# Kernel optimization log

Hardware: AMD Instinct MI355X
Metric: run time of the kernel (lower is better)

## Reference

```python
import jax, jax.numpy as jnp
import numpy as np

B, N, D, H, DH, E, BIAS_DIM = 8, 512, 512, 8, 64, 32768, 8

def setup_inputs() -> dict:
    key = jax.random.key(0)
    ks = jax.random.split(key, 10)
    states = jax.random.normal(ks[0], (B, N, D), jnp.float32)
    key_states = jax.random.normal(ks[1], (B, N, D), jnp.float32)
    # causal mask, broadcastable over heads: [B,1,N,N]
    masks = jnp.broadcast_to(jnp.tril(jnp.ones((N, N), jnp.float32)), (B, 1, N, N))
    edge_type = jax.random.randint(ks[2], (E, 1), 0, BIAS_DIM, jnp.int32)
    b_idx = jax.random.randint(ks[3], (E, 1), 0, B, jnp.int32)
    q_idx = jax.random.randint(ks[4], (E, 1), 0, N, jnp.int32)
    k_idx = jax.random.randint(ks[5], (E, 1), 0, N, jnp.int32)
    attention_bias = jnp.concatenate([edge_type, b_idx, q_idx, k_idx], axis=1)
    s = 0.05
    Wq = jax.random.normal(ks[6], (D, H, DH), jnp.float32) * s
    Wk = jax.random.normal(ks[7], (D, H, DH), jnp.float32) * s
    Wv = jax.random.normal(ks[8], (D, H, DH), jnp.float32) * s
    k2 = jax.random.split(ks[9], 3)
    Wo = jax.random.normal(k2[0], (H, DH, D), jnp.float32) * s
    bias_embs = jax.random.normal(k2[1], (BIAS_DIM, DH), jnp.float32) * s
    bias_scalar = jax.random.normal(k2[2], (DH, 1), jnp.float32) * s
    return {"states": states, "key_states": key_states, "masks": masks,
            "attention_bias": attention_bias, "Wq": Wq, "Wk": Wk, "Wv": Wv,
            "Wo": Wo, "bias_embs": bias_embs, "bias_scalar": bias_scalar}

def reference(states, key_states, masks, attention_bias, Wq, Wk, Wv, Wo, bias_embs, bias_scalar):
    q = jnp.einsum('btd,dha->btha', states, Wq)
    k = jnp.einsum('btd,dha->btha', key_states, Wk)
    v = jnp.einsum('btd,dha->btha', key_states, Wv)
    alpha = jnp.einsum('bkha,bqha->bhqk', k, q)  # [B,H,Q,K]
    # sparse edge bias: embed edge types, project to scalar, scatter into [B,Q,K]
    et = attention_bias[:, 0]
    bias_vals = (bias_embs[et] @ bias_scalar)[:, 0]  # [E]
    bq, bk = alpha.shape[2], alpha.shape[3]
    bias_mat = jnp.zeros((alpha.shape[0], bq, bk), alpha.dtype)
    bias_mat = bias_mat.at[attention_bias[:, 1], attention_bias[:, 2], attention_bias[:, 3]].add(bias_vals)
    summed_keys = jnp.sum(k, axis=-1)  # [B,K,H]
    alpha = alpha + jnp.einsum('bqk,bkh->bhqk', bias_mat, summed_keys)
    alpha = alpha * jax.lax.rsqrt(jnp.float32(DH))
    neg = jnp.finfo(jnp.float32).min
    alpha = alpha * masks + (1.0 - jnp.ceil(masks)) * neg
    alpha = jax.nn.softmax(alpha, axis=-1)
    alpha = alpha * masks
    context = jnp.einsum('bhqk,bkha->bqha', alpha, v)
    return jnp.einsum('btha,had->btd', context, Wo)
```

## Files before the change

kernel.cpp:

```cpp
#include <hip/hip_runtime.h>

typedef unsigned short u16;
typedef unsigned int u32;
typedef __bf16 bf16x8 __attribute__((ext_vector_type(8)));
typedef float f32x4 __attribute__((ext_vector_type(4)));
typedef u16 u16x8 __attribute__((ext_vector_type(8)));
typedef u16 u16x4 __attribute__((ext_vector_type(4)));


__device__ __forceinline__ u16 f2b(float f) {
  union { float f; u32 i; } v; v.f = f;
  u32 r = v.i + 0x7fffu + ((v.i >> 16) & 1u);
  return (u16)(r >> 16);
}

#define GLL16(gp, lp)                                                      \
  __builtin_amdgcn_global_load_lds(                                       \
      (const __attribute__((address_space(1))) u32*)(gp),                 \
      (__attribute__((address_space(3))) u32*)(lp), 16, 0, 0)

__device__ __forceinline__ void stage64(const u16* g, u16* l, int wave, int lane) {
  int rsub = lane >> 3;
  int gs = (((lane & 7) ^ rsub) << 3);
  #pragma unroll
  for (int c = 0; c < 2; c++) {
    int ch = wave * 2 + c;
    GLL16(g + (size_t)(ch * 8 + rsub) * 512 + gs, l + ch * 512);
  }
}
__device__ __forceinline__ void stage128(const u16* g, u16* l, int wave, int lane) {
  int rsub = lane >> 3;
  int gs = (((lane & 7) ^ rsub) << 3);
  #pragma unroll
  for (int c = 0; c < 4; c++) {
    int ch = wave * 4 + c;
    GLL16(g + (size_t)(ch * 8 + rsub) * 512 + gs, l + ch * 512);
  }
}
__device__ __forceinline__ int swz(int row, int g) {
  return row * 64 + ((g ^ (row & 7)) << 3);
}

__global__ __launch_bounds__(256) void wprep(
    const float* __restrict__ Wq, const float* __restrict__ Wk,
    const float* __restrict__ Wv, const float* __restrict__ Wo,
    u16* __restrict__ wbase, float* __restrict__ bias_mat) {
  __shared__ u16 t[32][33];
  int bid = blockIdx.x;
  int tid = threadIdx.x;
  if (bid < 1024) {
    int z = bid >> 8, rem = bid & 255;
    int bx = rem & 15, by = rem >> 4;
    const float* src; float sc = 1.f;
    if (z == 0)      { src = Wq; sc = 0.125f; }
    else if (z == 1) { src = Wk; }
    else if (z == 2) { src = Wv; }
    else             { src = Wo; }
    u16* dst = wbase + (size_t)z * 262144;
    int tx = tid & 31, ty = tid >> 5;
    int c0 = bx * 32, r0 = by * 32;
    #pragma unroll
    for (int i = ty; i < 32; i += 8) t[i][tx] = f2b(src[(r0 + i) * 512 + c0 + tx] * sc);
    __syncthreads();
    #pragma unroll
    for (int i = ty; i < 32; i += 8) dst[(c0 + i) * 512 + r0 + tx] = t[tx][i];
  } else {
    int i = (bid - 1024) * 256 + tid;
    float4 z4 = {0.f, 0.f, 0.f, 0.f};
    ((float4*)bias_mat)[i] = z4;
  }
}

__global__ __launch_bounds__(256) void qkv_gemm(const float* __restrict__ states,
                                                const float* __restrict__ key_states,
                                                const u16* __restrict__ wT,
                                                const int* __restrict__ ab,
                                                const float* __restrict__ be,
                                                const float* __restrict__ bsc,
                                                float* __restrict__ bias_m,
                                                u16* __restrict__ qb,
                                                u16* __restrict__ kbo,
                                                u16* __restrict__ vtb,
                                                float* __restrict__ summed,
                                                int n_edges) {
  __shared__ alignas(16) u16 As[2][64 * 64];
  __shared__ alignas(16) u16 Bs[2][128 * 64];
  __shared__ float ssum[4][64];
  __shared__ float tvs[8];
  int tid = threadIdx.x;
  int lane = tid & 63, wave = tid >> 6;
  int quad = lane >> 4, ln = lane & 15;
  int fb = blockIdx.y * 64 + blockIdx.x;

  if (tid < 8) {
    const float4* bev = (const float4*)(be + tid * 64);
    const float4* bscv = (const float4*)bsc;
    float s = 0.f;
    #pragma unroll
    for (int a4 = 0; a4 < 16; a4++) {
      float4 x = bev[a4], y = bscv[a4];
      s += x.x * y.x + x.y * y.y + x.z * y.z + x.w * y.w;
    }
    tvs[tid] = s * 0.125f;
  }
  __syncthreads();
  for (int e = fb * 256 + tid; e < n_edges; e += 768 * 256) {
    int et = ab[e * 4 + 0];
    int b  = ab[e * 4 + 1];
    int qi = ab[e * 4 + 2];
    int ki = ab[e * 4 + 3];
    if (ki <= qi)
      atomicAdd(&bias_m[((size_t)b * 512 + qi) * 512 + ki], tvs[et]);
  }

  int row0 = blockIdx.x * 64;
  int col0 = blockIdx.y * 128;
  const float* A = (col0 < 512) ? states : key_states;
  const u16* Bb = wT + (size_t)col0 * 512;

  int ar = tid >> 2, aj = tid & 3;
  const float* apA = A + (size_t)(row0 + ar) * 512 + aj * 16;

  f32x4 acc[4][2];
  #pragma unroll
  for (int i = 0; i < 4; i++)
    #pragma unroll
    for (int j = 0; j < 2; j++) acc[i][j] = (f32x4){0.f, 0.f, 0.f, 0.f};

  float4 rA[4];
  {
    const float4* p = (const float4*)apA;
    rA[0] = p[0]; rA[1] = p[1]; rA[2] = p[2]; rA[3] = p[3];
  }
  stage128(Bb, Bs[0], wave, lane);

  int cur = 0;
  for (int k0 = 0; k0 < 512; k0 += 64) {
    __syncthreads();
    {
      u16x8 q0, q1;
      q0[0]=f2b(rA[0].x); q0[1]=f2b(rA[0].y); q0[2]=f2b(rA[0].z); q0[3]=f2b(rA[0].w);
      q0[4]=f2b(rA[1].x); q0[5]=f2b(rA[1].y); q0[6]=f2b(rA[1].z); q0[7]=f2b(rA[1].w);
      q1[0]=f2b(rA[2].x); q1[1]=f2b(rA[2].y); q1[2]=f2b(rA[2].z); q1[3]=f2b(rA[2].w);
      q1[4]=f2b(rA[3].x); q1[5]=f2b(rA[3].y); q1[6]=f2b(rA[3].z); q1[7]=f2b(rA[3].w);
      *(u16x8*)&As[cur][swz(ar, 2 * aj)]     = q0;
      *(u16x8*)&As[cur][swz(ar, 2 * aj + 1)] = q1;
    }
    __syncthreads();
    if (k0 < 448) {
      stage128(Bb + k0 + 64, Bs[cur ^ 1], wave, lane);
      const float4* p = (const float4*)(apA + k0 + 64);
      rA[0] = p[0]; rA[1] = p[1]; rA[2] = p[2]; rA[3] = p[3];
    }
    #pragma unroll
    for (int s = 0; s < 2; s++) {
      bf16x8 af[4], bfv[2];
      #pragma unroll
      for (int i = 0; i < 4; i++)
        af[i] = *(bf16x8*)&As[cur][swz(i * 16 + ln, s * 4 + quad)];
      #pragma unroll
      for (int j = 0; j < 2; j++)
        bfv[j] = *(bf16x8*)&Bs[cur][swz(wave * 32 + j * 16 + ln, s * 4 + quad)];
      #pragma unroll
      for (int i = 0; i < 4; i++)
        #pragma unroll
        for (int j = 0; j < 2; j++)
          acc[i][j] = __builtin_amdgcn_mfma_f32_16x16x32_bf16(af[i], bfv[j], acc[i][j], 0, 0, 0);
    }
    cur ^= 1;
  }

  int region = col0 >> 9;
  int nbase = col0 & 511;
  if (region <= 1) {
    u16* Cout = region ? kbo : qb;
    #pragma unroll
    for (int i = 0; i < 4; i++)
      #pragma unroll
      for (int j = 0; j < 2; j++) {
        int mb = row0 + i * 16 + quad * 4;
        int n = nbase + wave * 32 + j * 16 + ln;
        #pragma unroll
        for (int r = 0; r < 4; r++)
          Cout[(size_t)(mb + r) * 512 + n] = f2b(acc[i][j][r]);
      }
    if (region == 1) {
      #pragma unroll
      for (int i = 0; i < 4; i++)
        #pragma unroll
        for (int r = 0; r < 4; r++) {
          float v = acc[i][0][r] + acc[i][1][r];
          v += __shfl_xor(v, 1);
          v += __shfl_xor(v, 2);
          v += __shfl_xor(v, 4);
          v += __shfl_xor(v, 8);
          if (ln == 0) ssum[wave][i * 16 + quad * 4 + r] = v;
        }
      __syncthreads();
      if (tid < 128) {
        int hl = tid >> 6, row = tid & 63;
        float s = ssum[hl * 2][row] + ssum[hl * 2 + 1][row];
        int m = row0 + row;
        int b = m >> 9, t = m & 511;
        int h = (nbase >> 6) + hl;
        summed[((size_t)(b * 8 + h)) * 512 + t] = s;
      }
    }
  } else {
    #pragma unroll
    for (int i = 0; i < 4; i++)
      #pragma unroll
      for (int j = 0; j < 2; j++) {
        int mb = row0 + i * 16 + quad * 4;
        int bb = mb >> 9, t0 = mb & 511;
        int a_abs = nbase + wave * 32 + j * 16 + ln;
        int h = a_abs >> 6, a = a_abs & 63;
        u16x4 p;
        p[0] = f2b(acc[i][j][0]); p[1] = f2b(acc[i][j][1]);
        p[2] = f2b(acc[i][j][2]); p[3] = f2b(acc[i][j][3]);
        *(u16x4*)&vtb[(((size_t)bb * 8 + h) * 64 + a) * 512 + t0] = p;
      }
  }
}

__global__ __launch_bounds__(256) void attn_mfma(const u16* __restrict__ q,
                                                 const u16* __restrict__ k,
                                                 const u16* __restrict__ vt,
                                                 const float* __restrict__ bias_mat,
                                                 const float* __restrict__ summed,
                                                 u16* __restrict__ ctx) {
  __shared__ alignas(16) u16 Qs[64 * 64];
  __shared__ alignas(16) u16 Ks[2][64 * 64];
  __shared__ alignas(16) u16 Vs[2][64 * 64];
  __shared__ alignas(16) u16 Ps[4][16 * 72];
  int tid = threadIdx.x;
  int wave = tid >> 6, lane = tid & 63;
  int quad = lane >> 4, ln = lane & 15;
  int p2 = blockIdx.x;
  int bh, qt;
  if (p2 < 256) { bh = p2 & 63; qt = 7 - (p2 >> 6); }
  else          { int q2 = p2 - 256; bh = q2 & 63; qt = q2 >> 6; }
  int b = bh >> 3, h = bh & 7;
  int q0 = qt * 64;
  int kbe = qt;

  const u16* qb_ = q + ((size_t)(b * 512 + q0)) * 512 + h * 64;
  const u16* kb_ = k + ((size_t)(b * 512)) * 512 + h * 64;
  const u16* vb_ = vt + ((size_t)bh * 64) * 512;

  stage64(qb_, Qs, wave, lane);
  stage64(kb_, Ks[0], wave, lane);
  stage64(vb_, Vs[0], wave, lane);

  float m_r[4], l_r[4];
  f32x4 o[4];
  #pragma unroll
  for (int r = 0; r < 4; r++) { m_r[r] = -3.40282347e38f; l_r[r] = 0.f; }
  #pragma unroll
  for (int nt = 0; nt < 4; nt++) o[nt] = (f32x4){0.f, 0.f, 0.f, 0.f};

  int qrow = q0 + wave * 16 + quad * 4;

  float c_skv[4], c_bias[4][4];
  #pragma unroll
  for (int nt = 0; nt < 4; nt++) {
    int t = nt * 16 + ln;
    c_skv[nt] = summed[bh * 512 + t];
    const float* bp2 = bias_mat + ((size_t)(b * 512 + qrow)) * 512 + t;
    #pragma unroll
    for (int r = 0; r < 4; r++) c_bias[nt][r] = bp2[(size_t)r * 512];
  }

  int cur = 0;
  for (int kb = 0; kb <= kbe; kb++) {
    __syncthreads();

    float n_skv[4], n_bias[4][4];
    if (kb < kbe) {
      stage64(kb_ + (size_t)(kb + 1) * 64 * 512, Ks[cur ^ 1], wave, lane);
      stage64(vb_ + (kb + 1) * 64, Vs[cur ^ 1], wave, lane);
      #pragma unroll
      for (int nt = 0; nt < 4; nt++) {
        int t = (kb + 1) * 64 + nt * 16 + ln;
        n_skv[nt] = summed[bh * 512 + t];
        const float* bp2 = bias_mat + ((size_t)(b * 512 + qrow)) * 512 + t;
        #pragma unroll
        for (int r = 0; r < 4; r++) n_bias[nt][r] = bp2[(size_t)r * 512];
      }
    }

    bf16x8 aq0 = *(bf16x8*)&Qs[swz(wave * 16 + ln, quad)];
    bf16x8 aq1 = *(bf16x8*)&Qs[swz(wave * 16 + ln, 4 + quad)];
    f32x4 s[4];
    #pragma unroll
    for (int nt = 0; nt < 4; nt++) {
      bf16x8 b0 = *(bf16x8*)&Ks[cur][swz(nt * 16 + ln, quad)];
      bf16x8 b1 = *(bf16x8*)&Ks[cur][swz(nt * 16 + ln, 4 + quad)];
      s[nt] = (f32x4){0.f, 0.f, 0.f, 0.f};
      s[nt] = __builtin_amdgcn_mfma_f32_16x16x32_bf16(aq0, b0, s[nt], 0, 0, 0);
      s[nt] = __builtin_amdgcn_mfma_f32_16x16x32_bf16(aq1, b1, s[nt], 0, 0, 0);
    }

    #pragma unroll
    for (int nt = 0; nt < 4; nt++) {
      int t = kb * 64 + nt * 16 + ln;
      #pragma unroll
      for (int r = 0; r < 4; r++) {
        float val = s[nt][r] + c_bias[nt][r] * c_skv[nt];
        s[nt][r] = (t <= qrow + r) ? val : -3.40282347e38f;
      }
    }

    float alpha[4];
    #pragma unroll
    for (int r = 0; r < 4; r++) {
      float tm = fmaxf(fmaxf(s[0][r], s[1][r]), fmaxf(s[2][r], s[3][r]));
      #pragma unroll
      for (int off = 8; off; off >>= 1) tm = fmaxf(tm, __shfl_xor(tm, off));
      float mn = fmaxf(m_r[r], tm);
      alpha[r] = __expf(m_r[r] - mn);
      m_r[r] = mn;
      float rs = 0.f;
      #pragma unroll
      for (int nt = 0; nt < 4; nt++) {
        float pp = __expf(s[nt][r] - mn);
        s[nt][r] = pp;
        rs += pp;
      }
      #pragma unroll
      for (int off = 8; off; off >>= 1) rs += __shfl_xor(rs, off);
      l_r[r] = l_r[r] * alpha[r] + rs;
    }

    #pragma unroll
    for (int nt = 0; nt < 4; nt++)
      #pragma unroll
      for (int r = 0; r < 4; r++)
        Ps[wave][(quad * 4 + r) * 72 + nt * 16 + ln] = f2b(s[nt][r]);
    #pragma unroll
    for (int nt = 0; nt < 4; nt++)
      #pragma unroll
      for (int r = 0; r < 4; r++)
        o[nt][r] *= alpha[r];

    bf16x8 ap0 = *(bf16x8*)&Ps[wave][ln * 72 + quad * 8];
    bf16x8 ap1 = *(bf16x8*)&Ps[wave][ln * 72 + 32 + quad * 8];
    #pragma unroll
    for (int nt = 0; nt < 4; nt++) {
      bf16x8 b0 = *(bf16x8*)&Vs[cur][swz(nt * 16 + ln, quad)];
      bf16x8 b1 = *(bf16x8*)&Vs[cur][swz(nt * 16 + ln, 4 + quad)];
      o[nt] = __builtin_amdgcn_mfma_f32_16x16x32_bf16(ap0, b0, o[nt], 0, 0, 0);
      o[nt] = __builtin_amdgcn_mfma_f32_16x16x32_bf16(ap1, b1, o[nt], 0, 0, 0);
    }

    if (kb < kbe) {
      #pragma unroll
      for (int nt = 0; nt < 4; nt++) {
        c_skv[nt] = n_skv[nt];
        #pragma unroll
        for (int r = 0; r < 4; r++) c_bias[nt][r] = n_bias[nt][r];
      }
    }
    cur ^= 1;
  }

  #pragma unroll
  for (int r = 0; r < 4; r++) {
    float inv = 1.f / l_r[r];
    int qr2 = qrow + r;
    u16* dst = ctx + ((size_t)(b * 512 + qr2)) * 512 + h * 64;
    #pragma unroll
    for (int nt = 0; nt < 4; nt++)
      dst[nt * 16 + ln] = f2b(o[nt][r] * inv);
  }
}

__global__ __launch_bounds__(256) void out_gemm(const u16* __restrict__ A,
                                                const u16* __restrict__ BT,
                                                float* __restrict__ C) {
  __shared__ alignas(16) u16 As[2][64 * 64];
  __shared__ alignas(16) u16 Bs[2][64 * 64];
  int tid = threadIdx.x;
  int lane = tid & 63, wave = tid >> 6;
  int quad = lane >> 4, ln = lane & 15;
  int wr = wave >> 1, wc = wave & 1;
  int row0 = blockIdx.x * 64;
  int col0 = blockIdx.y * 64;
  const u16* Ab = A + (size_t)row0 * 512;
  const u16* Bb = BT + (size_t)col0 * 512;

  f32x4 acc[2][2];
  #pragma unroll
  for (int i = 0; i < 2; i++)
    #pragma unroll
    for (int j = 0; j < 2; j++) acc[i][j] = (f32x4){0.f, 0.f, 0.f, 0.f};

  stage64(Ab, As[0], wave, lane);
  stage64(Bb, Bs[0], wave, lane);

  int cur = 0;
  for (int k0 = 0; k0 < 512; k0 += 64) {
    __syncthreads();
    if (k0 < 448) {
      stage64(Ab + k0 + 64, As[cur ^ 1], wave, lane);
      stage64(Bb + k0 + 64, Bs[cur ^ 1], wave, lane);
    }
    #pragma unroll
    for (int s = 0; s < 2; s++) {
      bf16x8 af[2], bfv[2];
      #pragma unroll
      for (int i = 0; i < 2; i++)
        af[i] = *(bf16x8*)&As[cur][swz(wr * 32 + i * 16 + ln, s * 4 + quad)];
      #pragma unroll
      for (int j = 0; j < 2; j++)
        bfv[j] = *(bf16x8*)&Bs[cur][swz(wc * 32 + j * 16 + ln, s * 4 + quad)];
      #pragma unroll
      for (int i = 0; i < 2; i++)
        #pragma unroll
        for (int j = 0; j < 2; j++)
          acc[i][j] = __builtin_amdgcn_mfma_f32_16x16x32_bf16(af[i], bfv[j], acc[i][j], 0, 0, 0);
    }
    cur ^= 1;
  }
  #pragma unroll
  for (int i = 0; i < 2; i++)
    #pragma unroll
    for (int j = 0; j < 2; j++) {
      int mb = row0 + wr * 32 + i * 16 + quad * 4;
      int n = col0 + wc * 32 + j * 16 + ln;
      #pragma unroll
      for (int r = 0; r < 4; r++)
        C[(size_t)(mb + r) * 512 + n] = acc[i][j][r];
    }
}

extern "C" void kernel_launch(void* const* d_in, const int* in_sizes, int n_in,
                              void* d_out, int out_size, void* d_ws, size_t ws_size,
                              hipStream_t stream) {
  const float* states     = (const float*)d_in[0];
  const float* key_states = (const float*)d_in[1];
  const int*   ab         = (const int*)d_in[3];
  const float* Wq         = (const float*)d_in[4];
  const float* Wk         = (const float*)d_in[5];
  const float* Wv         = (const float*)d_in[6];
  const float* Wo         = (const float*)d_in[7];
  const float* be         = (const float*)d_in[8];
  const float* bsc        = (const float*)d_in[9];
  float* out = (float*)d_out;

  char* ws = (char*)d_ws;
  const size_t MB = 1024 * 1024;
  u16* wbase    = (u16*)(ws);
  u16* wot      = (u16*)(ws + 1536 * 1024);
  u16* qb       = (u16*)(ws + 2 * MB);
  u16* kbo      = (u16*)(ws + 6 * MB);
  u16* vtb      = (u16*)(ws + 10 * MB);
  u16* ctxb     = (u16*)(ws + 14 * MB);
  float* bias_m = (float*)(ws + 18 * MB);
  float* summed = (float*)(ws + 26 * MB);

  int n_edges = in_sizes[3] / 4;

  wprep<<<dim3(3072), 256, 0, stream>>>(Wq, Wk, Wv, Wo, wbase, bias_m);
  qkv_gemm<<<dim3(64, 12), 256, 0, stream>>>(
      states, key_states, wbase, ab, be, bsc, bias_m, qb, kbo, vtb, summed, n_edges);
  attn_mfma<<<dim3(512), 256, 0, stream>>>(qb, kbo, vtb, bias_m, summed, ctxb);
  out_gemm<<<dim3(64, 8), 256, 0, stream>>>(ctxb, wot, out);
}
```

Before: 130.9 us.

## Fuse weight transpose and bf16 conversion into GEMM loaders, drop wprep kernel

Removes the separate weight-prep kernel that transposed and converted Wq/Wk/Wv/Wo to bf16 each call. The QKV and output GEMMs now load fp32 weights directly into registers with strided column reads, convert and scale them, and write them swizzled into LDS. The bias matrix is zeroed with hipMemsetAsync instead. This saves one launch and a weight round-trip, but replaces async global-to-LDS copies with synchronous register staging and adds an extra barrier in out_gemm. It also makes every GEMM block redo the weight conversion.

```diff
diff --git a/kernel.cpp b/kernel.cpp
--- a/kernel.cpp
+++ b/kernel.cpp
@@ -28,52 +28,15 @@
     GLL16(g + (size_t)(ch * 8 + rsub) * 512 + gs, l + ch * 512);
   }
 }
-__device__ __forceinline__ void stage128(const u16* g, u16* l, int wave, int lane) {
-  int rsub = lane >> 3;
-  int gs = (((lane & 7) ^ rsub) << 3);
-  #pragma unroll
-  for (int c = 0; c < 4; c++) {
-    int ch = wave * 4 + c;
-    GLL16(g + (size_t)(ch * 8 + rsub) * 512 + gs, l + ch * 512);
-  }
-}
 __device__ __forceinline__ int swz(int row, int g) {
   return row * 64 + ((g ^ (row & 7)) << 3);
 }
 
-__global__ __launch_bounds__(256) void wprep(
-    const float* __restrict__ Wq, const float* __restrict__ Wk,
-    const float* __restrict__ Wv, const float* __restrict__ Wo,
-    u16* __restrict__ wbase, float* __restrict__ bias_mat) {
-  __shared__ u16 t[32][33];
-  int bid = blockIdx.x;
-  int tid = threadIdx.x;
-  if (bid < 1024) {
-    int z = bid >> 8, rem = bid & 255;
-    int bx = rem & 15, by = rem >> 4;
-    const float* src; float sc = 1.f;
-    if (z == 0)      { src = Wq; sc = 0.125f; }
-    else if (z == 1) { src = Wk; }
-    else if (z == 2) { src = Wv; }
-    else             { src = Wo; }
-    u16* dst = wbase + (size_t)z * 262144;
-    int tx = tid & 31, ty = tid >> 5;
-    int c0 = bx * 32, r0 = by * 32;
-    #pragma unroll
-    for (int i = ty; i < 32; i += 8) t[i][tx] = f2b(src[(r0 + i) * 512 + c0 + tx] * sc);
-    __syncthreads();
-    #pragma unroll
-    for (int i = ty; i < 32; i += 8) dst[(c0 + i) * 512 + r0 + tx] = t[tx][i];
-  } else {
-    int i = (bid - 1024) * 256 + tid;
-    float4 z4 = {0.f, 0.f, 0.f, 0.f};
-    ((float4*)bias_mat)[i] = z4;
-  }
-}
-
 __global__ __launch_bounds__(256) void qkv_gemm(const float* __restrict__ states,
                                                 const float* __restrict__ key_states,
-                                                const u16* __restrict__ wT,
+                                                const float* __restrict__ Wq,
+                                                const float* __restrict__ Wk,
+                                                const float* __restrict__ Wv,
                                                 const int* __restrict__ ab,
                                                 const float* __restrict__ be,
                                                 const float* __restrict__ bsc,
@@ -115,11 +78,16 @@
 
   int row0 = blockIdx.x * 64;
   int col0 = blockIdx.y * 128;
-  const float* A = (col0 < 512) ? states : key_states;
-  const u16* Bb = wT + (size_t)col0 * 512;
+  int region = col0 >> 9;
+  int co = col0 & 511;
+  const float* A = (region == 0) ? states : key_states;
+  const float* Wz = (region == 0) ? Wq : (region == 1 ? Wk : Wv);
+  float sc = (region == 0) ? 0.125f : 1.f;
 
   int ar = tid >> 2, aj = tid & 3;
   const float* apA = A + (size_t)(row0 + ar) * 512 + aj * 16;
+  int bc = tid & 127, bh = tid >> 7;
+  const float* apB = Wz + (size_t)bh * 32 * 512 + co + bc;
 
   f32x4 acc[4][2];
   #pragma unroll
@@ -128,11 +96,13 @@
     for (int j = 0; j < 2; j++) acc[i][j] = (f32x4){0.f, 0.f, 0.f, 0.f};
 
   float4 rA[4];
+  float rB[32];
   {
     const float4* p = (const float4*)apA;
     rA[0] = p[0]; rA[1] = p[1]; rA[2] = p[2]; rA[3] = p[3];
-  }
-  stage128(Bb, Bs[0], wave, lane);
+    #pragma unroll
+    for (int i = 0; i < 32; i++) rB[i] = apB[(size_t)i * 512];
+  }
 
   int cur = 0;
   for (int k0 = 0; k0 < 512; k0 += 64) {
@@ -146,11 +116,20 @@
       *(u16x8*)&As[cur][swz(ar, 2 * aj)]     = q0;
       *(u16x8*)&As[cur][swz(ar, 2 * aj + 1)] = q1;
     }
+    #pragma unroll
+    for (int g2 = 0; g2 < 4; g2++) {
+      u16x8 pk;
+      #pragma unroll
+      for (int e8 = 0; e8 < 8; e8++) pk[e8] = f2b(rB[g2 * 8 + e8] * sc);
+      *(u16x8*)&Bs[cur][swz(bc, bh * 4 + g2)] = pk;
+    }
     __syncthreads();
     if (k0 < 448) {
-      stage128(Bb + k0 + 64, Bs[cur ^ 1], wave, lane);
       const float4* p = (const float4*)(apA + k0 + 64);
       rA[0] = p[0]; rA[1] = p[1]; rA[2] = p[2]; rA[3] = p[3];
+      const float* bp = apB + (size_t)(k0 + 64) * 512;
+      #pragma unroll
+      for (int i = 0; i < 32; i++) rB[i] = bp[(size_t)i * 512];
     }
     #pragma unroll
     for (int s = 0; s < 2; s++) {
@@ -170,8 +149,7 @@
     cur ^= 1;
   }
 
-  int region = col0 >> 9;
-  int nbase = col0 & 511;
+  int nbase = co;
   if (region <= 1) {
     u16* Cout = region ? kbo : qb;
     #pragma unroll
@@ -376,7 +354,7 @@
 }
 
 __global__ __launch_bounds__(256) void out_gemm(const u16* __restrict__ A,
-                                                const u16* __restrict__ BT,
+                                                const float* __restrict__ Wo,
                                                 float* __restrict__ C) {
   __shared__ alignas(16) u16 As[2][64 * 64];
   __shared__ alignas(16) u16 Bs[2][64 * 64];
@@ -387,7 +365,8 @@
   int row0 = blockIdx.x * 64;
   int col0 = blockIdx.y * 64;
   const u16* Ab = A + (size_t)row0 * 512;
-  const u16* Bb = BT + (size_t)col0 * 512;
+  int bc2 = tid & 63, bq = tid >> 6;
+  const float* apB = Wo + (size_t)bq * 16 * 512 + col0 + bc2;
 
   f32x4 acc[2][2];
   #pragma unroll
@@ -395,15 +374,27 @@
     #pragma unroll
     for (int j = 0; j < 2; j++) acc[i][j] = (f32x4){0.f, 0.f, 0.f, 0.f};
 
+  float rB[16];
+  #pragma unroll
+  for (int i = 0; i < 16; i++) rB[i] = apB[(size_t)i * 512];
   stage64(Ab, As[0], wave, lane);
-  stage64(Bb, Bs[0], wave, lane);
 
   int cur = 0;
   for (int k0 = 0; k0 < 512; k0 += 64) {
     __syncthreads();
+    #pragma unroll
+    for (int g2 = 0; g2 < 2; g2++) {
+      u16x8 pk;
+      #pragma unroll
+      for (int e8 = 0; e8 < 8; e8++) pk[e8] = f2b(rB[g2 * 8 + e8]);
+      *(u16x8*)&Bs[cur][swz(bc2, bq * 2 + g2)] = pk;
+    }
+    __syncthreads();
     if (k0 < 448) {
       stage64(Ab + k0 + 64, As[cur ^ 1], wave, lane);
-      stage64(Bb + k0 + 64, Bs[cur ^ 1], wave, lane);
+      const float* bp = apB + (size_t)(k0 + 64) * 512;
+      #pragma unroll
+      for (int i = 0; i < 16; i++) rB[i] = bp[(size_t)i * 512];
     }
     #pragma unroll
     for (int s = 0; s < 2; s++) {
@@ -450,20 +441,19 @@
 
   char* ws = (char*)d_ws;
   const size_t MB = 1024 * 1024;
-  u16* wbase    = (u16*)(ws);
-  u16* wot      = (u16*)(ws + 1536 * 1024);
-  u16* qb       = (u16*)(ws + 2 * MB);
-  u16* kbo      = (u16*)(ws + 6 * MB);
-  u16* vtb      = (u16*)(ws + 10 * MB);
-  u16* ctxb     = (u16*)(ws + 14 * MB);
-  float* bias_m = (float*)(ws + 18 * MB);
-  float* summed = (float*)(ws + 26 * MB);
+  u16* qb       = (u16*)(ws);
+  u16* kbo      = (u16*)(ws + 4 * MB);
+  u16* vtb      = (u16*)(ws + 8 * MB);
+  u16* ctxb     = (u16*)(ws + 12 * MB);
+  float* bias_m = (float*)(ws + 16 * MB);
+  float* summed = (float*)(ws + 24 * MB);
 
   int n_edges = in_sizes[3] / 4;
 
-  wprep<<<dim3(3072), 256, 0, stream>>>(Wq, Wk, Wv, Wo, wbase, bias_m);
+  hipMemsetAsync(bias_m, 0, (size_t)8 * MB, stream);
   qkv_gemm<<<dim3(64, 12), 256, 0, stream>>>(
-      states, key_states, wbase, ab, be, bsc, bias_m, qb, kbo, vtb, summed, n_edges);
+      states, key_states, Wq, Wk, Wv, ab, be, bsc, bias_m,
+      qb, kbo, vtb, summed, n_edges);
   attn_mfma<<<dim3(512), 256, 0, stream>>>(qb, kbo, vtb, bias_m, summed, ctxb);
-  out_gemm<<<dim3(64, 8), 256, 0, stream>>>(ctxb, wot, out);
-}
+  out_gemm<<<dim3(64, 8), 256, 0, stream>>>(ctxb, Wo, out);
+}
```

Result: slower. 137.2 us (+4.8%).
